# Performance work log

Measured on AMD Instinct MI355X. Metric: run time of the kernel, lower is better.

The kernel has to match this reference:

```python
import jax, jax.numpy as jnp
import numpy as np

T = 3
B, N, F = 8, 256, 32
E_DIM = 8
HID = 32
IN_DIM = 2 * (F + 1) + E_DIM  # 74


def setup_inputs() -> dict:
    key = jax.random.key(0)
    ks = jax.random.split(key, 10)
    h = jax.random.normal(ks[0], (B, N, F), dtype=jnp.float32)
    e = jax.random.uniform(ks[1], (B, N, N, E_DIM), dtype=jnp.float32)
    q = jax.random.normal(ks[2], (B, N, 1), dtype=jnp.float32)
    mask = jnp.ones((B, N), dtype=jnp.float32)
    s1 = 1.0 / np.sqrt(IN_DIM)
    s2 = 1.0 / np.sqrt(HID)
    W1 = jax.random.normal(ks[3], (T, IN_DIM, HID), dtype=jnp.float32) * s1
    b1 = jnp.zeros((T, HID), dtype=jnp.float32)
    W2 = jax.random.normal(ks[4], (T, HID, HID), dtype=jnp.float32) * s2
    b2 = jnp.zeros((T, HID), dtype=jnp.float32)
    W3 = jax.random.normal(ks[5], (T, HID, 1), dtype=jnp.float32) * s2
    b3 = jnp.zeros((T, 1), dtype=jnp.float32)
    return {"h": h, "e": e, "q": q, "mask": mask,
            "W1": W1, "b1": b1, "W2": W2, "b2": b2, "W3": W3, "b3": b3}


def reference(h, e, q, mask, W1, b1, W2, b2, W3, b3):
    tol = jnp.float32(1e-8)
    clip = jnp.clip(e, tol, 1e5)
    largest_e = jnp.max(clip, axis=-1)          # [B,N,N]
    is_near = (largest_e != tol).astype(h.dtype)
    m = mask.astype(h.dtype)
    exp_mask = m[:, :, None] * m[:, None, :]    # [B,N,N]
    natom = e.shape[1]

    def mlp(x, t):
        x = jax.nn.relu(jnp.matmul(x, W1[t]) + b1[t])
        x = jax.nn.relu(jnp.matmul(x, W2[t]) + b2[t])
        return (jnp.matmul(x, W3[t]) + b3[t])[..., 0]  # [B,N,N]

    for t in range(T):
        inp = jnp.concatenate([h, q], axis=-1)  # [B,N,F+1]
        d = inp.shape[-1]
        inp_i = jnp.broadcast_to(inp[:, :, None, :], (inp.shape[0], natom, natom, d))
        inp_j = jnp.broadcast_to(inp[:, None, :, :], (inp.shape[0], natom, natom, d))
        inp_ij = jnp.concatenate([inp_i, inp_j, e], axis=-1)  # [B,N,N,IN_DIM]
        inp_ji = jnp.concatenate([inp_j, inp_i, e], axis=-1)
        elec_ij = mlp(inp_ij, t)
        elec_ji = mlp(inp_ji, t)
        antisym = 0.5 * (elec_ij - elec_ji) * exp_mask * is_near
        q = q + jnp.sum(antisym, axis=2)[..., None]
    return q
```

## Files before the change

kernel.cpp:

```cpp
#include <hip/hip_runtime.h>
#include <hip/hip_bf16.h>


typedef __attribute__((ext_vector_type(8))) short short8;
typedef __attribute__((ext_vector_type(4))) short short4v;
typedef __attribute__((ext_vector_type(4))) float f32x4;
union U4S8 { uint4 u; short8 s; };
union U2S4 { uint2 u; short4v s; };
#define F4(p) (*(const float4*)(p))

#if defined(__HIP_DEVICE_COMPILE__)
# if __has_builtin(__builtin_amdgcn_mfma_f32_16x16x16bf16_1k)
#  define MFMA16(a,b,c) __builtin_amdgcn_mfma_f32_16x16x16bf16_1k(a,b,c,0,0,0)
# elif __has_builtin(__builtin_amdgcn_mfma_f32_16x16x16_bf16)
#  define MFMA16(a,b,c) __builtin_amdgcn_mfma_f32_16x16x16_bf16(a,b,c,0,0,0)
# else
#  error "no 16x16x16 bf16 MFMA builtin on this target"
# endif
#else
# define MFMA16(a,b,c) (f32x4{0.f,0.f,0.f,0.f})
#endif

__device__ __forceinline__ unsigned pkbf2(float lo, float hi) {
    unsigned a = __bfloat16_as_ushort(__float2bfloat16(lo));
    unsigned b = __bfloat16_as_ushort(__float2bfloat16(hi));
    return a | (b << 16);
}
__device__ __forceinline__ float bf2f(unsigned short u) {
    return __uint_as_float(((unsigned)u) << 16);
}

__global__ __launch_bounds__(256) void epn_pre(
    const float* __restrict__ h, const float* __restrict__ W1,
    const float* __restrict__ b1, const float* __restrict__ W2,
    unsigned short* __restrict__ basePbf, unsigned short* __restrict__ baseQbf,
    uint2* __restrict__ W2T16, uint4* __restrict__ WA)
{
    const int t  = blockIdx.x >> 8;
    const int lg = (blockIdx.x & 255) * 256 + threadIdx.x;
    const float* W1t = W1 + t*2368;
    if (lg < 256) {
        int f = lg >> 6, lane = lg & 63;
        int kh = f >> 1, nt = f & 1;
        int sl = lane >> 4, l15 = lane & 15;
        int k0 = kh*16 + sl*4, n = nt*16 + l15;
        const float* W2t = W2 + t*1024;
        W2T16[t*256 + lg] = make_uint2(
            pkbf2(W2t[k0*32 + n],     W2t[(k0+1)*32 + n]),
            pkbf2(W2t[(k0+2)*32 + n], W2t[(k0+3)*32 + n]));
    } else if (lg < 384) {
        int g2 = lg - 256;
        int kt = g2 >> 6, lane = g2 & 63;
        int l15 = lane & 15, sl = lane >> 4;
        float v[8];
        #pragma unroll
        for (int p = 0; p < 8; ++p) {
            int d = sl*8 + p;
            v[p] = (d < 8) ? W1t[(66+d)*32 + kt*16 + l15]
                           : ((kt*16 + l15 == d - 8) ? 1.0f : 0.0f);
        }
        WA[t*128 + g2] = make_uint4(pkbf2(v[0],v[1]), pkbf2(v[2],v[3]),
                                    pkbf2(v[4],v[5]), pkbf2(v[6],v[7]));
    }
    const int node = lg >> 5, k = lg & 31;
    const float* hn = h + node*32;
    float p = b1[t*32 + k], qq = 0.f;
    #pragma unroll
    for (int f = 0; f < 32; ++f) {
        float hv = hn[f];
        p  += hv * W1t[f*32 + k];
        qq += hv * W1t[(33+f)*32 + k];
    }
    basePbf[t*65536 + lg] = __bfloat16_as_ushort(__float2bfloat16(p));
    baseQbf[t*65536 + lg] = __bfloat16_as_ushort(__float2bfloat16(qq));
}

__global__ __launch_bounds__(256, 4) void epn_main(
    const float* __restrict__ e, const float* __restrict__ mask,
    const uint4* __restrict__ bP4, const uint4* __restrict__ bQ4,
    const float* __restrict__ qrowP, const float* __restrict__ qrowQ,
    const uint2* __restrict__ W2T16, const uint4* __restrict__ WA,
    const float* __restrict__ b2, const float* __restrict__ W3,
    const float* __restrict__ q_src, float* __restrict__ q_dst)
{
    __shared__ uint4 sx[9][256];
    __shared__ float mnL[256];
    __shared__ float red[4];

    const int bi = blockIdx.x, b = bi >> 8;
    const int tid = threadIdx.x, j = tid;
    const int lane = tid & 63, w = tid >> 6;
    const int l15 = lane & 15, sl = lane >> 4;

    float qj = q_src[b*256 + j];
    unsigned qpk = __bfloat16_as_ushort(__float2bfloat16(qj));
    const float* ejp = e + ((size_t)bi*256 + j)*8;
    float4 e0 = F4(ejp), e1 = F4(ejp + 4);
    float mx = fmaxf(fmaxf(fmaxf(e0.x,e0.y),fmaxf(e0.z,e0.w)),
                     fmaxf(fmaxf(e1.x,e1.y),fmaxf(e1.z,e1.w)));
    float nearf = (fminf(fmaxf(mx, 1e-8f), 1e5f) != 1e-8f) ? 1.f : 0.f;
    mnL[j] = mask[bi] * mask[b*256 + j] * nearf;
    sx[0][j] = make_uint4(pkbf2(e0.x,e0.y), pkbf2(e0.z,e0.w),
                          pkbf2(e1.x,e1.y), pkbf2(e1.z,e1.w));
    {
        const uint4* bq = bQ4 + (size_t)(b*256 + j)*4;
        const uint4* bp = bP4 + (size_t)(b*256 + j)*4;
        sx[1][j]=bq[0]; sx[2][j]=bq[1]; sx[3][j]=bq[2]; sx[4][j]=bq[3];
        sx[5][j]=bp[0]; sx[6][j]=bp[1]; sx[7][j]=bp[2]; sx[8][j]=bp[3];
    }

    U4S8 wa00, wa01, wa1;
    wa00.u = WA[lane];
    wa01.u = WA[64 + lane];
    wa1.u  = make_uint4(0u,0u,0u,0u);
    if (sl == 0 && l15 >= 8) {
        int p = l15 - 8;
        unsigned v = 0x3F80u << ((p & 1) * 16);
        wa1.u.x = ((p>>1)==0)?v:0u;  wa1.u.y = ((p>>1)==1)?v:0u;
        wa1.u.z = ((p>>1)==2)?v:0u;  wa1.u.w = ((p>>1)==3)?v:0u;
    }
    unsigned aqQ0 = 0, aqQ1 = 0, aqP0 = 0, aqP1 = 0;
    if (sl == 0) {
        aqQ0 = __bfloat16_as_ushort(__float2bfloat16(qrowQ[l15]));
        aqQ1 = __bfloat16_as_ushort(__float2bfloat16(qrowQ[16 + l15]));
        aqP0 = __bfloat16_as_ushort(__float2bfloat16(qrowP[l15]));
        aqP1 = __bfloat16_as_ushort(__float2bfloat16(qrowP[16 + l15]));
    }
    float qi = q_src[bi];
    const unsigned short* bPi = (const unsigned short*)bP4 + (size_t)bi*32;
    const unsigned short* bQi = (const unsigned short*)bQ4 + (size_t)bi*32;
    f32x4 ckP0, ckP1, ckQ0, ckQ1;
    #pragma unroll
    for (int r = 0; r < 4; ++r) {
        int k0 = sl*4 + r, k1 = 16 + sl*4 + r;
        ckP0[r] = bf2f(bPi[k0]) + qi * qrowP[k0];
        ckP1[r] = bf2f(bPi[k1]) + qi * qrowP[k1];
        ckQ0[r] = bf2f(bQi[k0]) + qi * qrowQ[k0];
        ckQ1[r] = bf2f(bQi[k1]) + qi * qrowQ[k1];
    }
    U2S4 bu00, bu10, bu01, bu11;
    bu00.u = W2T16[0*64 + lane];
    bu01.u = W2T16[1*64 + lane];
    bu10.u = W2T16[2*64 + lane];
    bu11.u = W2T16[3*64 + lane];
    float b2v0 = b2[l15], b2v1 = b2[l15+16];
    float w3v0 = W3[l15], w3v1 = W3[l15+16];
    const int slot0_d0 = (sl == 0) ? 0 : sl;
    const int slot0_d1 = (sl == 0) ? 0 : 4 + sl;

    float tot = 0.f;
    #pragma unroll
    for (int rt = 0; rt < 4; ++rt) {
        const int rl  = rt*16 + l15;
        const int row = w*64 + rl;
        unsigned qr = __shfl(qpk, rl);
        U4S8 bc2; bc2.u = make_uint4((sl == 0) ? (qr & 0xFFFFu) : 0u, 0u, 0u, 0u);
        float pA[4], pB[4];
        #pragma unroll
        for (int dir = 0; dir < 2; ++dir) {
            U4S8 bc0, bc1, aq0, aq1;
            bc0.u = sx[dir ? slot0_d1 : slot0_d0][row];
            bc1.u = sx[dir ? 8 : 4][row];
            aq0.u = make_uint4(dir ? aqP0 : aqQ0, 0u, 0u, 0u);
            aq1.u = make_uint4(dir ? aqP1 : aqQ1, 0u, 0u, 0u);
            f32x4 c0 = dir ? ckQ0 : ckP0;
            f32x4 c1 = dir ? ckQ1 : ckP1;
            f32x4 dk0 = __builtin_amdgcn_mfma_f32_16x16x32_bf16(wa00.s, bc0.s, c0, 0,0,0);
            dk0 = __builtin_amdgcn_mfma_f32_16x16x32_bf16(aq0.s, bc2.s, dk0, 0,0,0);
            f32x4 dk1 = __builtin_amdgcn_mfma_f32_16x16x32_bf16(wa01.s, bc0.s, c1, 0,0,0);
            dk1 = __builtin_amdgcn_mfma_f32_16x16x32_bf16(wa1.s,  bc1.s, dk1, 0,0,0);
            dk1 = __builtin_amdgcn_mfma_f32_16x16x32_bf16(aq1.s,  bc2.s, dk1, 0,0,0);
            U2S4 a0, a1;
            a0.u = make_uint2(pkbf2(fmaxf(dk0[0],0.f), fmaxf(dk0[1],0.f)),
                              pkbf2(fmaxf(dk0[2],0.f), fmaxf(dk0[3],0.f)));
            a1.u = make_uint2(pkbf2(fmaxf(dk1[0],0.f), fmaxf(dk1[1],0.f)),
                              pkbf2(fmaxf(dk1[2],0.f), fmaxf(dk1[3],0.f)));
            f32x4 z = {0.f, 0.f, 0.f, 0.f};
            f32x4 d0 = MFMA16(a0.s, bu00.s, z);
            d0 = MFMA16(a1.s, bu10.s, d0);
            f32x4 d1 = MFMA16(a0.s, bu01.s, z);
            d1 = MFMA16(a1.s, bu11.s, d1);
            float* pp = dir ? pB : pA;
            pp[0] = fmaxf(d0[0]+b2v0,0.f)*w3v0 + fmaxf(d1[0]+b2v1,0.f)*w3v1;
            pp[1] = fmaxf(d0[1]+b2v0,0.f)*w3v0 + fmaxf(d1[1]+b2v1,0.f)*w3v1;
            pp[2] = fmaxf(d0[2]+b2v0,0.f)*w3v0 + fmaxf(d1[2]+b2v1,0.f)*w3v1;
            pp[3] = fmaxf(d0[3]+b2v0,0.f)*w3v0 + fmaxf(d1[3]+b2v1,0.f)*w3v1;
        }
        float4 mr = *(const float4*)&mnL[w*64 + rt*16 + sl*4];
        tot += mr.x*(pA[0]-pB[0]) + mr.y*(pA[1]-pB[1])
             + mr.z*(pA[2]-pB[2]) + mr.w*(pA[3]-pB[3]);
    }
    #pragma unroll
    for (int off = 32; off > 0; off >>= 1) tot += __shfl_down(tot, off);
    if (lane == 0) red[w] = tot;
    __syncthreads();
    if (tid == 0)
        q_dst[bi] = q_src[bi] + 0.5f * (red[0] + red[1] + red[2] + red[3]);
}

extern "C" void kernel_launch(void* const* d_in, const int* in_sizes, int n_in,
                              void* d_out, int out_size, void* d_ws, size_t ws_size,
                              hipStream_t stream) {
    (void)in_sizes; (void)n_in; (void)out_size; (void)ws_size;
    const float* h    = (const float*)d_in[0];
    const float* e    = (const float*)d_in[1];
    const float* q    = (const float*)d_in[2];
    const float* mask = (const float*)d_in[3];
    const float* W1   = (const float*)d_in[4];
    const float* b1   = (const float*)d_in[5];
    const float* W2   = (const float*)d_in[6];
    const float* b2   = (const float*)d_in[7];
    const float* W3   = (const float*)d_in[8];

    char* ws = (char*)d_ws;
    unsigned short* basePbf = (unsigned short*)ws;
    unsigned short* baseQbf = (unsigned short*)(ws + 393216);
    float* qA   = (float*)(ws + 786432);
    float* qB   = (float*)(ws + 794624);
    uint2* W2T16 = (uint2*)(ws + 802816);
    uint4* WA    = (uint4*)(ws + 808960);

    epn_pre<<<768, 256, 0, stream>>>(h, W1, b1, W2, basePbf, baseQbf, W2T16, WA);

    const float* qsrc = q;
    for (int t = 0; t < 3; ++t) {
        float* qdst = (t == 2) ? (float*)d_out : (t == 0 ? qA : qB);
        epn_main<<<2048, 256, 0, stream>>>(
            e, mask,
            (const uint4*)(basePbf + t*65536), (const uint4*)(baseQbf + t*65536),
            W1 + t*2368 + 32*32, W1 + t*2368 + 65*32,
            W2T16 + t*256, WA + t*128,
            b2 + t*32, W3 + t*32, qsrc, qdst);
        qsrc = qdst;
    }
}
```

Baseline: 52.75 us.

## Process two i-rows per block to reuse staged j-feature tiles

Each block now handles two consecutive atoms i instead of one, and the grid is halved. The per-j bf16 base projections are staged in shared memory once and reused for both rows. Both rows' e tiles are loaded up front, and the per-row bias and edge work is recomputed inside a two-iteration loop with a separate reduction for each. This cuts redundant global and shared-memory staging traffic and per-block setup, at the cost of fewer blocks and longer serial work per block.

```diff
diff --git a/kernel.cpp b/kernel.cpp
--- a/kernel.cpp
+++ b/kernel.cpp
@@ -83,31 +83,35 @@
     const float* __restrict__ b2, const float* __restrict__ W3,
     const float* __restrict__ q_src, float* __restrict__ q_dst)
 {
-    __shared__ uint4 sx[9][256];
+    __shared__ uint4 sxJ[8][256];
+    __shared__ uint4 se[256];
     __shared__ float mnL[256];
-    __shared__ float red[4];
-
-    const int bi = blockIdx.x, b = bi >> 8;
+    __shared__ float red[8];
+
+    const int bid = blockIdx.x;
+    const int b   = bid >> 7;
+    const int bi0 = b*256 + (bid & 127)*2;
     const int tid = threadIdx.x, j = tid;
     const int lane = tid & 63, w = tid >> 6;
     const int l15 = lane & 15, sl = lane >> 4;
 
-    float qj = q_src[b*256 + j];
-    unsigned qpk = __bfloat16_as_ushort(__float2bfloat16(qj));
-    const float* ejp = e + ((size_t)bi*256 + j)*8;
-    float4 e0 = F4(ejp), e1 = F4(ejp + 4);
-    float mx = fmaxf(fmaxf(fmaxf(e0.x,e0.y),fmaxf(e0.z,e0.w)),
-                     fmaxf(fmaxf(e1.x,e1.y),fmaxf(e1.z,e1.w)));
-    float nearf = (fminf(fmaxf(mx, 1e-8f), 1e5f) != 1e-8f) ? 1.f : 0.f;
-    mnL[j] = mask[bi] * mask[b*256 + j] * nearf;
-    sx[0][j] = make_uint4(pkbf2(e0.x,e0.y), pkbf2(e0.z,e0.w),
-                          pkbf2(e1.x,e1.y), pkbf2(e1.z,e1.w));
     {
         const uint4* bq = bQ4 + (size_t)(b*256 + j)*4;
         const uint4* bp = bP4 + (size_t)(b*256 + j)*4;
-        sx[1][j]=bq[0]; sx[2][j]=bq[1]; sx[3][j]=bq[2]; sx[4][j]=bq[3];
-        sx[5][j]=bp[0]; sx[6][j]=bp[1]; sx[7][j]=bp[2]; sx[8][j]=bp[3];
-    }
+        sxJ[0][j]=bq[0]; sxJ[1][j]=bq[1]; sxJ[2][j]=bq[2]; sxJ[3][j]=bq[3];
+        sxJ[4][j]=bp[0]; sxJ[5][j]=bp[1]; sxJ[6][j]=bp[2]; sxJ[7][j]=bp[3];
+    }
+    float maskj = mask[b*256 + j];
+    float qj = q_src[b*256 + j];
+    unsigned qpk = __bfloat16_as_ushort(__float2bfloat16(qj));
+    unsigned qr_rt[4];
+    #pragma unroll
+    for (int rt = 0; rt < 4; ++rt) qr_rt[rt] = __shfl(qpk, rt*16 + l15);
+
+    const float* ej0 = e + ((size_t)bi0*256 + j)*8;
+    const float* ej1 = e + ((size_t)(bi0+1)*256 + j)*8;
+    float4 e00 = F4(ej0), e01 = F4(ej0 + 4);
+    float4 e10 = F4(ej1), e11 = F4(ej1 + 4);
 
     U4S8 wa00, wa01, wa1;
     wa00.u = WA[lane];
@@ -126,18 +130,6 @@
         aqP0 = __bfloat16_as_ushort(__float2bfloat16(qrowP[l15]));
         aqP1 = __bfloat16_as_ushort(__float2bfloat16(qrowP[16 + l15]));
     }
-    float qi = q_src[bi];
-    const unsigned short* bPi = (const unsigned short*)bP4 + (size_t)bi*32;
-    const unsigned short* bQi = (const unsigned short*)bQ4 + (size_t)bi*32;
-    f32x4 ckP0, ckP1, ckQ0, ckQ1;
-    #pragma unroll
-    for (int r = 0; r < 4; ++r) {
-        int k0 = sl*4 + r, k1 = 16 + sl*4 + r;
-        ckP0[r] = bf2f(bPi[k0]) + qi * qrowP[k0];
-        ckP1[r] = bf2f(bPi[k1]) + qi * qrowP[k1];
-        ckQ0[r] = bf2f(bQi[k0]) + qi * qrowQ[k0];
-        ckQ1[r] = bf2f(bQi[k1]) + qi * qrowQ[k1];
-    }
     U2S4 bu00, bu10, bu01, bu11;
     bu00.u = W2T16[0*64 + lane];
     bu01.u = W2T16[1*64 + lane];
@@ -145,57 +137,93 @@
     bu11.u = W2T16[3*64 + lane];
     float b2v0 = b2[l15], b2v1 = b2[l15+16];
     float w3v0 = W3[l15], w3v1 = W3[l15+16];
+    float qrP0v[4], qrP1v[4], qrQ0v[4], qrQ1v[4];
+    #pragma unroll
+    for (int r = 0; r < 4; ++r) {
+        qrP0v[r] = qrowP[sl*4 + r];  qrP1v[r] = qrowP[16 + sl*4 + r];
+        qrQ0v[r] = qrowQ[sl*4 + r];  qrQ1v[r] = qrowQ[16 + sl*4 + r];
+    }
     const int slot0_d0 = (sl == 0) ? 0 : sl;
     const int slot0_d1 = (sl == 0) ? 0 : 4 + sl;
 
-    float tot = 0.f;
-    #pragma unroll
-    for (int rt = 0; rt < 4; ++rt) {
-        const int rl  = rt*16 + l15;
-        const int row = w*64 + rl;
-        unsigned qr = __shfl(qpk, rl);
-        U4S8 bc2; bc2.u = make_uint4((sl == 0) ? (qr & 0xFFFFu) : 0u, 0u, 0u, 0u);
-        float pA[4], pB[4];
+    #pragma unroll
+    for (int p = 0; p < 2; ++p) {
+        const int bi = bi0 + p;
+        float4 ea = p ? e10 : e00;
+        float4 eb = p ? e11 : e01;
+        float mx = fmaxf(fmaxf(fmaxf(ea.x,ea.y),fmaxf(ea.z,ea.w)),
+                         fmaxf(fmaxf(eb.x,eb.y),fmaxf(eb.z,eb.w)));
+        float nearf = (fminf(fmaxf(mx, 1e-8f), 1e5f) != 1e-8f) ? 1.f : 0.f;
+        mnL[j] = mask[bi] * maskj * nearf;
+        se[j] = make_uint4(pkbf2(ea.x,ea.y), pkbf2(ea.z,ea.w),
+                           pkbf2(eb.x,eb.y), pkbf2(eb.z,eb.w));
+        float qi = q_src[bi];
+        const unsigned short* bPi = (const unsigned short*)bP4 + (size_t)bi*32;
+        const unsigned short* bQi = (const unsigned short*)bQ4 + (size_t)bi*32;
+        ushort4 bp0 = *(const ushort4*)(bPi + sl*4);
+        ushort4 bp1 = *(const ushort4*)(bPi + 16 + sl*4);
+        ushort4 bq0 = *(const ushort4*)(bQi + sl*4);
+        ushort4 bq1 = *(const ushort4*)(bQi + 16 + sl*4);
+        f32x4 ckP0 = {bf2f(bp0.x)+qi*qrP0v[0], bf2f(bp0.y)+qi*qrP0v[1],
+                      bf2f(bp0.z)+qi*qrP0v[2], bf2f(bp0.w)+qi*qrP0v[3]};
+        f32x4 ckP1 = {bf2f(bp1.x)+qi*qrP1v[0], bf2f(bp1.y)+qi*qrP1v[1],
+                      bf2f(bp1.z)+qi*qrP1v[2], bf2f(bp1.w)+qi*qrP1v[3]};
+        f32x4 ckQ0 = {bf2f(bq0.x)+qi*qrQ0v[0], bf2f(bq0.y)+qi*qrQ0v[1],
+                      bf2f(bq0.z)+qi*qrQ0v[2], bf2f(bq0.w)+qi*qrQ0v[3]};
+        f32x4 ckQ1 = {bf2f(bq1.x)+qi*qrQ1v[0], bf2f(bq1.y)+qi*qrQ1v[1],
+                      bf2f(bq1.z)+qi*qrQ1v[2], bf2f(bq1.w)+qi*qrQ1v[3]};
+
+        float tot = 0.f;
         #pragma unroll
-        for (int dir = 0; dir < 2; ++dir) {
-            U4S8 bc0, bc1, aq0, aq1;
-            bc0.u = sx[dir ? slot0_d1 : slot0_d0][row];
-            bc1.u = sx[dir ? 8 : 4][row];
-            aq0.u = make_uint4(dir ? aqP0 : aqQ0, 0u, 0u, 0u);
-            aq1.u = make_uint4(dir ? aqP1 : aqQ1, 0u, 0u, 0u);
-            f32x4 c0 = dir ? ckQ0 : ckP0;
-            f32x4 c1 = dir ? ckQ1 : ckP1;
-            f32x4 dk0 = __builtin_amdgcn_mfma_f32_16x16x32_bf16(wa00.s, bc0.s, c0, 0,0,0);
-            dk0 = __builtin_amdgcn_mfma_f32_16x16x32_bf16(aq0.s, bc2.s, dk0, 0,0,0);
-            f32x4 dk1 = __builtin_amdgcn_mfma_f32_16x16x32_bf16(wa01.s, bc0.s, c1, 0,0,0);
-            dk1 = __builtin_amdgcn_mfma_f32_16x16x32_bf16(wa1.s,  bc1.s, dk1, 0,0,0);
-            dk1 = __builtin_amdgcn_mfma_f32_16x16x32_bf16(aq1.s,  bc2.s, dk1, 0,0,0);
-            U2S4 a0, a1;
-            a0.u = make_uint2(pkbf2(fmaxf(dk0[0],0.f), fmaxf(dk0[1],0.f)),
-                              pkbf2(fmaxf(dk0[2],0.f), fmaxf(dk0[3],0.f)));
-            a1.u = make_uint2(pkbf2(fmaxf(dk1[0],0.f), fmaxf(dk1[1],0.f)),
-                              pkbf2(fmaxf(dk1[2],0.f), fmaxf(dk1[3],0.f)));
-            f32x4 z = {0.f, 0.f, 0.f, 0.f};
-            f32x4 d0 = MFMA16(a0.s, bu00.s, z);
-            d0 = MFMA16(a1.s, bu10.s, d0);
-            f32x4 d1 = MFMA16(a0.s, bu01.s, z);
-            d1 = MFMA16(a1.s, bu11.s, d1);
-            float* pp = dir ? pB : pA;
-            pp[0] = fmaxf(d0[0]+b2v0,0.f)*w3v0 + fmaxf(d1[0]+b2v1,0.f)*w3v1;
-            pp[1] = fmaxf(d0[1]+b2v0,0.f)*w3v0 + fmaxf(d1[1]+b2v1,0.f)*w3v1;
-            pp[2] = fmaxf(d0[2]+b2v0,0.f)*w3v0 + fmaxf(d1[2]+b2v1,0.f)*w3v1;
-            pp[3] = fmaxf(d0[3]+b2v0,0.f)*w3v0 + fmaxf(d1[3]+b2v1,0.f)*w3v1;
+        for (int rt = 0; rt < 4; ++rt) {
+            const int row = w*64 + rt*16 + l15;
+            U4S8 bc2; bc2.u = make_uint4((sl == 0) ? (qr_rt[rt] & 0xFFFFu) : 0u,
+                                         0u, 0u, 0u);
+            float pA[4], pB[4];
+            #pragma unroll
+            for (int dir = 0; dir < 2; ++dir) {
+                U4S8 bc0, bc1, aq0, aq1;
+                bc0.u = (sl == 0) ? se[row]
+                                  : sxJ[(dir ? slot0_d1 : slot0_d0) - 1 + (dir?-3:0)][row];
+                bc0.u = (sl == 0) ? se[row] : (dir ? sxJ[3 + sl][row] : sxJ[sl - 1][row]);
+                bc1.u = dir ? sxJ[7][row] : sxJ[3][row];
+                aq0.u = make_uint4(dir ? aqP0 : aqQ0, 0u, 0u, 0u);
+                aq1.u = make_uint4(dir ? aqP1 : aqQ1, 0u, 0u, 0u);
+                f32x4 c0v = dir ? ckQ0 : ckP0;
+                f32x4 c1v = dir ? ckQ1 : ckP1;
+                f32x4 dk0 = __builtin_amdgcn_mfma_f32_16x16x32_bf16(wa00.s, bc0.s, c0v, 0,0,0);
+                dk0 = __builtin_amdgcn_mfma_f32_16x16x32_bf16(aq0.s, bc2.s, dk0, 0,0,0);
+                f32x4 dk1 = __builtin_amdgcn_mfma_f32_16x16x32_bf16(wa01.s, bc0.s, c1v, 0,0,0);
+                dk1 = __builtin_amdgcn_mfma_f32_16x16x32_bf16(wa1.s,  bc1.s, dk1, 0,0,0);
+                dk1 = __builtin_amdgcn_mfma_f32_16x16x32_bf16(aq1.s,  bc2.s, dk1, 0,0,0);
+                U2S4 a0, a1;
+                a0.u = make_uint2(pkbf2(fmaxf(dk0[0],0.f), fmaxf(dk0[1],0.f)),
+                                  pkbf2(fmaxf(dk0[2],0.f), fmaxf(dk0[3],0.f)));
+                a1.u = make_uint2(pkbf2(fmaxf(dk1[0],0.f), fmaxf(dk1[1],0.f)),
+                                  pkbf2(fmaxf(dk1[2],0.f), fmaxf(dk1[3],0.f)));
+                f32x4 z = {0.f, 0.f, 0.f, 0.f};
+                f32x4 d0 = MFMA16(a0.s, bu00.s, z);
+                d0 = MFMA16(a1.s, bu10.s, d0);
+                f32x4 d1 = MFMA16(a0.s, bu01.s, z);
+                d1 = MFMA16(a1.s, bu11.s, d1);
+                float* pp = dir ? pB : pA;
+                pp[0] = fmaxf(d0[0]+b2v0,0.f)*w3v0 + fmaxf(d1[0]+b2v1,0.f)*w3v1;
+                pp[1] = fmaxf(d0[1]+b2v0,0.f)*w3v0 + fmaxf(d1[1]+b2v1,0.f)*w3v1;
+                pp[2] = fmaxf(d0[2]+b2v0,0.f)*w3v0 + fmaxf(d1[2]+b2v1,0.f)*w3v1;
+                pp[3] = fmaxf(d0[3]+b2v0,0.f)*w3v0 + fmaxf(d1[3]+b2v1,0.f)*w3v1;
+            }
+            float4 mr = *(const float4*)&mnL[w*64 + rt*16 + sl*4];
+            tot += mr.x*(pA[0]-pB[0]) + mr.y*(pA[1]-pB[1])
+                 + mr.z*(pA[2]-pB[2]) + mr.w*(pA[3]-pB[3]);
         }
-        float4 mr = *(const float4*)&mnL[w*64 + rt*16 + sl*4];
-        tot += mr.x*(pA[0]-pB[0]) + mr.y*(pA[1]-pB[1])
-             + mr.z*(pA[2]-pB[2]) + mr.w*(pA[3]-pB[3]);
-    }
-    #pragma unroll
-    for (int off = 32; off > 0; off >>= 1) tot += __shfl_down(tot, off);
-    if (lane == 0) red[w] = tot;
-    __syncthreads();
-    if (tid == 0)
-        q_dst[bi] = q_src[bi] + 0.5f * (red[0] + red[1] + red[2] + red[3]);
+        #pragma unroll
+        for (int off = 32; off > 0; off >>= 1) tot += __shfl_down(tot, off);
+        if (lane == 0) red[p*4 + w] = tot;
+        __syncthreads();
+        if (tid == 0)
+            q_dst[bi] = q_src[bi] + 0.5f*(red[p*4+0] + red[p*4+1]
+                                        + red[p*4+2] + red[p*4+3]);
+    }
 }
 
 extern "C" void kernel_launch(void* const* d_in, const int* in_sizes, int n_in,
@@ -215,8 +243,8 @@
     char* ws = (char*)d_ws;
     unsigned short* basePbf = (unsigned short*)ws;
     unsigned short* baseQbf = (unsigned short*)(ws + 393216);
-    float* qA   = (float*)(ws + 786432);
-    float* qB   = (float*)(ws + 794624);
+    float* qA    = (float*)(ws + 786432);
+    float* qB    = (float*)(ws + 794624);
     uint2* W2T16 = (uint2*)(ws + 802816);
     uint4* WA    = (uint4*)(ws + 808960);
 
@@ -225,7 +253,7 @@
     const float* qsrc = q;
     for (int t = 0; t < 3; ++t) {
         float* qdst = (t == 2) ? (float*)d_out : (t == 0 ? qA : qB);
-        epn_main<<<2048, 256, 0, stream>>>(
+        epn_main<<<1024, 256, 0, stream>>>(
             e, mask,
             (const uint4*)(basePbf + t*65536), (const uint4*)(baseQbf + t*65536),
             W1 + t*2368 + 32*32, W1 + t*2368 + 65*32,
```

Result: slower. 56.38 us (+6.9%).
